# Kernel tuning notes

Hardware: AMD Instinct MI355X
Metric: run time of the kernel (lower is better)

## Reference

```python
import jax, jax.numpy as jnp
import numpy as np

HIDDEN_DIM = 2048
NUM_EXPERTS = 64
TOP_K = 8
NUM_TOKENS = 16384


def setup_inputs() -> dict:
    key = jax.random.key(0)
    k_x, k_w, k_b = jax.random.split(key, 3)
    X = jax.random.normal(k_x, (NUM_TOKENS, HIDDEN_DIM), dtype=jnp.float32)
    # nn.Linear(hidden_dim, num_experts): weight [out, in], bias [out]
    bound = 1.0 / np.sqrt(HIDDEN_DIM)
    W_gate = jax.random.uniform(k_w, (NUM_EXPERTS, HIDDEN_DIM), jnp.float32, -bound, bound)
    b_gate = jax.random.uniform(k_b, (NUM_EXPERTS,), jnp.float32, -bound, bound)
    return {"X": X, "W_gate": W_gate, "b_gate": b_gate}


def reference(X, W_gate, b_gate):
    # gate linear: [T, H] @ [H, E] + [E] -> [T, E]
    router_logits = jnp.einsum('th,eh->te', X, W_gate) + b_gate
    # softmax in float32 (matches dtype=torch.float)
    router_probs = jax.nn.softmax(router_logits.astype(jnp.float32), axis=-1)
    # top-k over experts: [T, K]
    router_weights, selected_experts_indices = jax.lax.top_k(router_probs, TOP_K)
    router_weights = router_weights / jnp.sum(router_weights, axis=-1, keepdims=True)
    router_weights = router_weights.astype(X.dtype)
    # one-hot [T, K, E] -> permute(2,1,0) -> [E, K, T]
    expert_mask = jax.nn.one_hot(selected_experts_indices, NUM_EXPERTS, dtype=jnp.int64 if jax.config.jax_enable_x64 else jnp.int32)
    expert_mask = jnp.transpose(expert_mask, (2, 1, 0))
    return (router_logits, router_weights, selected_experts_indices.astype(jnp.int32), expert_mask)
```

## Files before the change

kernel.cpp:

```cpp
#include <hip/hip_runtime.h>

#define NT 16384
#define NH 2048
#define NE 64
#define TOPK 8
#define TT 64
#define KC 64
#define NCH (NH / KC)

#define LOFF 0
#define WOFF (NT * NE)
#define IOFF (WOFF + NT * TOPK)
#define MOFF (IOFF + NT * TOPK)

typedef __attribute__((ext_vector_type(8))) short short8;
typedef __attribute__((ext_vector_type(4))) float floatx4;

union FragU { uint4 u; short8 s; };

__device__ __forceinline__ unsigned pack3(float a, float b, unsigned& w1, unsigned& w2) {
    unsigned au = __float_as_uint(a), bu = __float_as_uint(b);
    unsigned ah0 = au & 0xFFFF0000u, bh0 = bu & 0xFFFF0000u;
    float ra = a - __uint_as_float(ah0);
    float rb = b - __uint_as_float(bh0);
    unsigned ar = __float_as_uint(ra), br = __float_as_uint(rb);
    unsigned ah1 = ar & 0xFFFF0000u, bh1 = br & 0xFFFF0000u;
    float sa = ra - __uint_as_float(ah1);
    float sb = rb - __uint_as_float(bh1);
    w1 = bh1 | (ah1 >> 16);
    w2 = (__float_as_uint(sb) & 0xFFFF0000u) | (__float_as_uint(sa) >> 16);
    return bh0 | (ah0 >> 16);
}

__global__ __launch_bounds__(512, 1)
void router_kernel(const float* __restrict__ X, const float* __restrict__ Wg,
                   const float* __restrict__ bg, float* __restrict__ out) {
    __shared__ unsigned short SP[2][6][64][64];
    __shared__ float P[64 * 64];
    __shared__ float Ls[TT][NE + 1];

    const int tid  = threadIdx.x;
    const int wave = tid >> 6;
    const int l    = tid & 63;
    const int tp = wave & 1, ep = (wave >> 1) & 1, kh = wave >> 2;
    const int tbase = blockIdx.x * TT;

    const int srow = tid >> 3;
    const int g8   = tid & 7;
    const int spg  = g8 ^ (srow & 7);
    const float* xrow = X  + (size_t)(tbase + srow) * NH + g8 * 8;
    const float* wrow = Wg + (size_t)srow * NH + g8 * 8;

    const int lr = l & 15, lq = l >> 4;

    floatx4 acc[2][2];
#pragma unroll
    for (int a = 0; a < 2; a++)
#pragma unroll
        for (int b = 0; b < 2; b++) acc[a][b] = (floatx4)0.0f;

    float4 xl0 = *(const float4*)(xrow);
    float4 xl1 = *(const float4*)(xrow + 4);
    float4 wl0 = *(const float4*)(wrow);
    float4 wl1 = *(const float4*)(wrow + 4);

    for (int k = 0; k < NCH; k++) {
        const int bsel = k & 1;
        unsigned xw1[4], xw2[4], ww1[4], ww2[4];
        uint4 x0, w0, x1, x2, w1v, w2v;
        x0.x = pack3(xl0.x, xl0.y, xw1[0], xw2[0]);
        x0.y = pack3(xl0.z, xl0.w, xw1[1], xw2[1]);
        x0.z = pack3(xl1.x, xl1.y, xw1[2], xw2[2]);
        x0.w = pack3(xl1.z, xl1.w, xw1[3], xw2[3]);
        w0.x = pack3(wl0.x, wl0.y, ww1[0], ww2[0]);
        w0.y = pack3(wl0.z, wl0.w, ww1[1], ww2[1]);
        w0.z = pack3(wl1.x, wl1.y, ww1[2], ww2[2]);
        w0.w = pack3(wl1.z, wl1.w, ww1[3], ww2[3]);
        x1 = make_uint4(xw1[0], xw1[1], xw1[2], xw1[3]);
        x2 = make_uint4(xw2[0], xw2[1], xw2[2], xw2[3]);
        w1v = make_uint4(ww1[0], ww1[1], ww1[2], ww1[3]);
        w2v = make_uint4(ww2[0], ww2[1], ww2[2], ww2[3]);
        *(uint4*)&SP[bsel][0][srow][spg * 8] = x0;
        *(uint4*)&SP[bsel][1][srow][spg * 8] = x1;
        *(uint4*)&SP[bsel][2][srow][spg * 8] = x2;
        *(uint4*)&SP[bsel][3][srow][spg * 8] = w0;
        *(uint4*)&SP[bsel][4][srow][spg * 8] = w1v;
        *(uint4*)&SP[bsel][5][srow][spg * 8] = w2v;
        __syncthreads();

        if (k + 1 < NCH) {
            const int go = (k + 1) * KC;
            xl0 = *(const float4*)(xrow + go);
            xl1 = *(const float4*)(xrow + go + 4);
            wl0 = *(const float4*)(wrow + go);
            wl1 = *(const float4*)(wrow + go + 4);
        }

        if ((k >> 4) == kh) {
#pragma unroll
            for (int s = 0; s < 2; s++) {
                short8 af[2][3], bf[2][3];
#pragma unroll
                for (int a = 0; a < 2; a++) {
                    const int row = (tp * 2 + a) * 16 + lr;
                    const int pgr = (s * 4 + lq) ^ (lr & 7);
#pragma unroll
                    for (int p = 0; p < 3; p++) {
                        FragU t; t.u = *(const uint4*)&SP[bsel][p][row][pgr * 8];
                        af[a][p] = t.s;
                    }
                }
#pragma unroll
                for (int b = 0; b < 2; b++) {
                    const int row = (ep * 2 + b) * 16 + lr;
                    const int pgr = (s * 4 + lq) ^ (lr & 7);
#pragma unroll
                    for (int p = 0; p < 3; p++) {
                        FragU t; t.u = *(const uint4*)&SP[bsel][3 + p][row][pgr * 8];
                        bf[b][p] = t.s;
                    }
                }
#pragma unroll
                for (int a = 0; a < 2; a++)
#pragma unroll
                    for (int b = 0; b < 2; b++) {
                        acc[a][b] = __builtin_amdgcn_mfma_f32_16x16x32_bf16(af[a][0], bf[b][0], acc[a][b], 0, 0, 0);
                        acc[a][b] = __builtin_amdgcn_mfma_f32_16x16x32_bf16(af[a][0], bf[b][1], acc[a][b], 0, 0, 0);
                        acc[a][b] = __builtin_amdgcn_mfma_f32_16x16x32_bf16(af[a][1], bf[b][0], acc[a][b], 0, 0, 0);
                        acc[a][b] = __builtin_amdgcn_mfma_f32_16x16x32_bf16(af[a][1], bf[b][1], acc[a][b], 0, 0, 0);
                        acc[a][b] = __builtin_amdgcn_mfma_f32_16x16x32_bf16(af[a][0], bf[b][2], acc[a][b], 0, 0, 0);
                        acc[a][b] = __builtin_amdgcn_mfma_f32_16x16x32_bf16(af[a][2], bf[b][0], acc[a][b], 0, 0, 0);
                    }
            }
        }
    }
    __syncthreads();

    if (kh == 1) {
#pragma unroll
        for (int a = 0; a < 2; a++)
#pragma unroll
            for (int b = 0; b < 2; b++)
#pragma unroll
                for (int r = 0; r < 4; r++) {
                    const int tok = (tp * 2 + a) * 16 + lq * 4 + r;
                    const int exp = (ep * 2 + b) * 16 + lr;
                    P[tok * 64 + exp] = acc[a][b][r];
                }
    }
    __syncthreads();

    if (kh == 0) {
#pragma unroll
        for (int b = 0; b < 2; b++) {
            const int exp = (ep * 2 + b) * 16 + lr;
            const float bias = bg[exp];
#pragma unroll
            for (int a = 0; a < 2; a++)
#pragma unroll
                for (int r = 0; r < 4; r++) {
                    const int tok = (tp * 2 + a) * 16 + lq * 4 + r;
                    Ls[tok][exp] = acc[a][b][r] + P[tok * 64 + exp] + bias;
                }
        }
    } else {
        float4 z = make_float4(0.f, 0.f, 0.f, 0.f);
        for (int m = tid - 256; m < 8192; m += 256) {
            int seg = m >> 4;
            int off = (m & 15) << 2;
            *(float4*)(out + MOFF + (size_t)seg * NT + tbase + off) = z;
        }
    }
    __syncthreads();

#pragma unroll
    for (int v = 0; v < 2; v++) {
        int f  = v * 512 + tid;
        int t  = f >> 4;
        int c4 = (f & 15) << 2;
        float4 o = make_float4(Ls[t][c4], Ls[t][c4 + 1], Ls[t][c4 + 2], Ls[t][c4 + 3]);
        *(float4*)(out + LOFF + (size_t)(tbase + t) * NE + c4) = o;
    }

    if (tid < TT) {
        const int t = tid;
        const size_t gt = (size_t)(tbase + t);

        float m = -1e30f;
#pragma unroll
        for (int e = 0; e < NE; e++) m = fmaxf(m, Ls[t][e]);

        unsigned long long sel = 0ULL;
        int   idxs[TOPK];
        float vals[TOPK];
#pragma unroll
        for (int kk = 0; kk < TOPK; kk++) {
            float best = -1e30f;
            int   bi   = 0;
            for (int e = 0; e < NE; e++) {
                if (!((sel >> e) & 1ULL)) {
                    float v = Ls[t][e];
                    if (v > best) { best = v; bi = e; }
                }
            }
            sel |= (1ULL << bi);
            idxs[kk] = bi;
            vals[kk] = best;
        }

        float ex[TOPK];
        float s = 0.0f;
#pragma unroll
        for (int kk = 0; kk < TOPK; kk++) { ex[kk] = __expf(vals[kk] - m); s += ex[kk]; }
        float inv = 1.0f / s;

#pragma unroll
        for (int kk = 0; kk < TOPK; kk++) {
            out[WOFF + gt * TOPK + kk] = ex[kk] * inv;
            out[IOFF + gt * TOPK + kk] = (float)idxs[kk];
            out[MOFF + (size_t)idxs[kk] * (TOPK * NT) + (size_t)kk * NT + gt] = 1.0f;
        }
    }
}

extern "C" void kernel_launch(void* const* d_in, const int* in_sizes, int n_in,
                              void* d_out, int out_size, void* d_ws, size_t ws_size,
                              hipStream_t stream) {
    const float* X  = (const float*)d_in[0];
    const float* Wg = (const float*)d_in[1];
    const float* bg = (const float*)d_in[2];
    float* out = (float*)d_out;

    hipLaunchKernelGGL(router_kernel, dim3(NT / TT), dim3(512), 0, stream,
                       X, Wg, bg, out);
}
```

Before: 238.1 us.

## Pre-split gate weights into bf16x3 fragments and load MFMA operands directly from global

Adds a small pre-kernel that converts W_gate once per call into MFMA-fragment-ordered bf16 triple-split form in workspace. The main kernel now uses 32-token blocks of 256 threads with a four-way K split. Each wave loads X and the pre-split W fragments straight from global into registers, with no LDS staging or per-chunk barriers, and reduces partial sums through shared memory. Top-k moves from a serial per-thread loop to 8-lane shuffle reductions. The cost is an extra kernel launch and heavier per-wave global traffic for W, which is shared across blocks and expected to hit in cache.

```diff
diff --git a/kernel.cpp b/kernel.cpp
--- a/kernel.cpp
+++ b/kernel.cpp
@@ -4,9 +4,11 @@
 #define NH 2048
 #define NE 64
 #define TOPK 8
-#define TT 64
-#define KC 64
-#define NCH (NH / KC)
+
+#define TB 32
+#define KSTEPS 64
+#define KQ 4
+#define KSW (KSTEPS / KQ)
 
 #define LOFF 0
 #define WOFF (NT * NE)
@@ -32,195 +34,183 @@
     return bh0 | (ah0 >> 16);
 }
 
-__global__ __launch_bounds__(512, 1)
-void router_kernel(const float* __restrict__ X, const float* __restrict__ Wg,
+__global__ __launch_bounds__(64)
+void wconv_kernel(const float* __restrict__ Wg, uint4* __restrict__ wsp) {
+    const int b = blockIdx.x;
+    const int t = b >> 2, g = b & 3;
+    const int l = threadIdx.x;
+    const int e  = g * 16 + (l & 15);
+    const int k0 = t * 32 + (l >> 4) * 8;
+    const float* src = Wg + (size_t)e * NH + k0;
+    float4 w0 = *(const float4*)src;
+    float4 w1 = *(const float4*)(src + 4);
+    unsigned u1[4], u2[4];
+    uint4 p0;
+    p0.x = pack3(w0.x, w0.y, u1[0], u2[0]);
+    p0.y = pack3(w0.z, w0.w, u1[1], u2[1]);
+    p0.z = pack3(w1.x, w1.y, u1[2], u2[2]);
+    p0.w = pack3(w1.z, w1.w, u1[3], u2[3]);
+    uint4* dst = wsp + (size_t)((t * 4 + g) * 3) * 64 + l;
+    dst[0]   = p0;
+    dst[64]  = make_uint4(u1[0], u1[1], u1[2], u1[3]);
+    dst[128] = make_uint4(u2[0], u2[1], u2[2], u2[3]);
+}
+
+__global__ __launch_bounds__(256, 2)
+void router_kernel(const float* __restrict__ X, const uint4* __restrict__ wsp,
                    const float* __restrict__ bg, float* __restrict__ out) {
-    __shared__ unsigned short SP[2][6][64][64];
-    __shared__ float P[64 * 64];
-    __shared__ float Ls[TT][NE + 1];
-
-    const int tid  = threadIdx.x;
-    const int wave = tid >> 6;
-    const int l    = tid & 63;
-    const int tp = wave & 1, ep = (wave >> 1) & 1, kh = wave >> 2;
-    const int tbase = blockIdx.x * TT;
-
-    const int srow = tid >> 3;
-    const int g8   = tid & 7;
-    const int spg  = g8 ^ (srow & 7);
-    const float* xrow = X  + (size_t)(tbase + srow) * NH + g8 * 8;
-    const float* wrow = Wg + (size_t)srow * NH + g8 * 8;
-
-    const int lr = l & 15, lq = l >> 4;
-
-    floatx4 acc[2][2];
+    __shared__ __align__(16) float P[KQ][TB][68];
+    __shared__ __align__(16) float Ls[TB][68];
+
+    const int tid = threadIdx.x;
+    const int kh  = tid >> 6;
+    const int l   = tid & 63;
+    const int lr  = l & 15, lq = l >> 4;
+    const int tbase = blockIdx.x * TB;
+
+    floatx4 acc[2][4];
 #pragma unroll
     for (int a = 0; a < 2; a++)
 #pragma unroll
-        for (int b = 0; b < 2; b++) acc[a][b] = (floatx4)0.0f;
-
-    float4 xl0 = *(const float4*)(xrow);
-    float4 xl1 = *(const float4*)(xrow + 4);
-    float4 wl0 = *(const float4*)(wrow);
-    float4 wl1 = *(const float4*)(wrow + 4);
-
-    for (int k = 0; k < NCH; k++) {
-        const int bsel = k & 1;
-        unsigned xw1[4], xw2[4], ww1[4], ww2[4];
-        uint4 x0, w0, x1, x2, w1v, w2v;
-        x0.x = pack3(xl0.x, xl0.y, xw1[0], xw2[0]);
-        x0.y = pack3(xl0.z, xl0.w, xw1[1], xw2[1]);
-        x0.z = pack3(xl1.x, xl1.y, xw1[2], xw2[2]);
-        x0.w = pack3(xl1.z, xl1.w, xw1[3], xw2[3]);
-        w0.x = pack3(wl0.x, wl0.y, ww1[0], ww2[0]);
-        w0.y = pack3(wl0.z, wl0.w, ww1[1], ww2[1]);
-        w0.z = pack3(wl1.x, wl1.y, ww1[2], ww2[2]);
-        w0.w = pack3(wl1.z, wl1.w, ww1[3], ww2[3]);
-        x1 = make_uint4(xw1[0], xw1[1], xw1[2], xw1[3]);
-        x2 = make_uint4(xw2[0], xw2[1], xw2[2], xw2[3]);
-        w1v = make_uint4(ww1[0], ww1[1], ww1[2], ww1[3]);
-        w2v = make_uint4(ww2[0], ww2[1], ww2[2], ww2[3]);
-        *(uint4*)&SP[bsel][0][srow][spg * 8] = x0;
-        *(uint4*)&SP[bsel][1][srow][spg * 8] = x1;
-        *(uint4*)&SP[bsel][2][srow][spg * 8] = x2;
-        *(uint4*)&SP[bsel][3][srow][spg * 8] = w0;
-        *(uint4*)&SP[bsel][4][srow][spg * 8] = w1v;
-        *(uint4*)&SP[bsel][5][srow][spg * 8] = w2v;
-        __syncthreads();
-
-        if (k + 1 < NCH) {
-            const int go = (k + 1) * KC;
-            xl0 = *(const float4*)(xrow + go);
-            xl1 = *(const float4*)(xrow + go + 4);
-            wl0 = *(const float4*)(wrow + go);
-            wl1 = *(const float4*)(wrow + go + 4);
-        }
-
-        if ((k >> 4) == kh) {
-#pragma unroll
-            for (int s = 0; s < 2; s++) {
-                short8 af[2][3], bf[2][3];
-#pragma unroll
-                for (int a = 0; a < 2; a++) {
-                    const int row = (tp * 2 + a) * 16 + lr;
-                    const int pgr = (s * 4 + lq) ^ (lr & 7);
-#pragma unroll
-                    for (int p = 0; p < 3; p++) {
-                        FragU t; t.u = *(const uint4*)&SP[bsel][p][row][pgr * 8];
-                        af[a][p] = t.s;
-                    }
-                }
-#pragma unroll
-                for (int b = 0; b < 2; b++) {
-                    const int row = (ep * 2 + b) * 16 + lr;
-                    const int pgr = (s * 4 + lq) ^ (lr & 7);
-#pragma unroll
-                    for (int p = 0; p < 3; p++) {
-                        FragU t; t.u = *(const uint4*)&SP[bsel][3 + p][row][pgr * 8];
-                        bf[b][p] = t.s;
-                    }
-                }
-#pragma unroll
-                for (int a = 0; a < 2; a++)
-#pragma unroll
-                    for (int b = 0; b < 2; b++) {
-                        acc[a][b] = __builtin_amdgcn_mfma_f32_16x16x32_bf16(af[a][0], bf[b][0], acc[a][b], 0, 0, 0);
-                        acc[a][b] = __builtin_amdgcn_mfma_f32_16x16x32_bf16(af[a][0], bf[b][1], acc[a][b], 0, 0, 0);
-                        acc[a][b] = __builtin_amdgcn_mfma_f32_16x16x32_bf16(af[a][1], bf[b][0], acc[a][b], 0, 0, 0);
-                        acc[a][b] = __builtin_amdgcn_mfma_f32_16x16x32_bf16(af[a][1], bf[b][1], acc[a][b], 0, 0, 0);
-                        acc[a][b] = __builtin_amdgcn_mfma_f32_16x16x32_bf16(af[a][0], bf[b][2], acc[a][b], 0, 0, 0);
-                        acc[a][b] = __builtin_amdgcn_mfma_f32_16x16x32_bf16(af[a][2], bf[b][0], acc[a][b], 0, 0, 0);
-                    }
+        for (int g = 0; g < 4; g++) acc[a][g] = (floatx4)0.0f;
+
+    const float* xp0 = X + (size_t)(tbase + lr) * NH + kh * (KSW * 32) + lq * 8;
+    const float* xp1 = xp0 + (size_t)16 * NH;
+    const uint4* wp = wsp + (size_t)(kh * KSW) * 12 * 64 + l;
+
+    float4 a0lo = *(const float4*)xp0;
+    float4 a0hi = *(const float4*)(xp0 + 4);
+    float4 a1lo = *(const float4*)xp1;
+    float4 a1hi = *(const float4*)(xp1 + 4);
+
+    {
+        float4 z = make_float4(0.f, 0.f, 0.f, 0.f);
+#pragma unroll
+        for (int m = 0; m < 16; m++) {
+            int f2  = tid + 256 * m;
+            int seg = f2 >> 3;
+            int off = (f2 & 7) << 2;
+            *(float4*)(out + MOFF + (size_t)seg * NT + tbase + off) = z;
+        }
+    }
+
+#pragma unroll 2
+    for (int t = 0; t < KSW; t++) {
+        FragU b[4][3];
+        const uint4* wt = wp + t * 768;
+#pragma unroll
+        for (int g = 0; g < 4; g++)
+#pragma unroll
+            for (int p = 0; p < 3; p++)
+                b[g][p].u = wt[(g * 3 + p) * 64];
+
+        FragU af[2][3];
+        {
+            unsigned u1[4], u2[4];
+            uint4 q;
+            q.x = pack3(a0lo.x, a0lo.y, u1[0], u2[0]);
+            q.y = pack3(a0lo.z, a0lo.w, u1[1], u2[1]);
+            q.z = pack3(a0hi.x, a0hi.y, u1[2], u2[2]);
+            q.w = pack3(a0hi.z, a0hi.w, u1[3], u2[3]);
+            af[0][0].u = q;
+            af[0][1].u = make_uint4(u1[0], u1[1], u1[2], u1[3]);
+            af[0][2].u = make_uint4(u2[0], u2[1], u2[2], u2[3]);
+            q.x = pack3(a1lo.x, a1lo.y, u1[0], u2[0]);
+            q.y = pack3(a1lo.z, a1lo.w, u1[1], u2[1]);
+            q.z = pack3(a1hi.x, a1hi.y, u1[2], u2[2]);
+            q.w = pack3(a1hi.z, a1hi.w, u1[3], u2[3]);
+            af[1][0].u = q;
+            af[1][1].u = make_uint4(u1[0], u1[1], u1[2], u1[3]);
+            af[1][2].u = make_uint4(u2[0], u2[1], u2[2], u2[3]);
+        }
+
+        if (t + 1 < KSW) {
+            const float* nx0 = xp0 + (t + 1) * 32;
+            const float* nx1 = xp1 + (t + 1) * 32;
+            a0lo = *(const float4*)nx0;
+            a0hi = *(const float4*)(nx0 + 4);
+            a1lo = *(const float4*)nx1;
+            a1hi = *(const float4*)(nx1 + 4);
+        }
+
+#pragma unroll
+        for (int g = 0; g < 4; g++)
+#pragma unroll
+            for (int a = 0; a < 2; a++) {
+                acc[a][g] = __builtin_amdgcn_mfma_f32_16x16x32_bf16(af[a][0].s, b[g][0].s, acc[a][g], 0, 0, 0);
+                acc[a][g] = __builtin_amdgcn_mfma_f32_16x16x32_bf16(af[a][0].s, b[g][1].s, acc[a][g], 0, 0, 0);
+                acc[a][g] = __builtin_amdgcn_mfma_f32_16x16x32_bf16(af[a][1].s, b[g][0].s, acc[a][g], 0, 0, 0);
+                acc[a][g] = __builtin_amdgcn_mfma_f32_16x16x32_bf16(af[a][1].s, b[g][1].s, acc[a][g], 0, 0, 0);
+                acc[a][g] = __builtin_amdgcn_mfma_f32_16x16x32_bf16(af[a][0].s, b[g][2].s, acc[a][g], 0, 0, 0);
+                acc[a][g] = __builtin_amdgcn_mfma_f32_16x16x32_bf16(af[a][2].s, b[g][0].s, acc[a][g], 0, 0, 0);
             }
-        }
-    }
+    }
+
+#pragma unroll
+    for (int a = 0; a < 2; a++)
+#pragma unroll
+        for (int g = 0; g < 4; g++)
+#pragma unroll
+            for (int r = 0; r < 4; r++)
+                P[kh][a * 16 + lq * 4 + r][g * 16 + lr] = acc[a][g][r];
     __syncthreads();
 
-    if (kh == 1) {
-#pragma unroll
-        for (int a = 0; a < 2; a++)
-#pragma unroll
-            for (int b = 0; b < 2; b++)
-#pragma unroll
-                for (int r = 0; r < 4; r++) {
-                    const int tok = (tp * 2 + a) * 16 + lq * 4 + r;
-                    const int exp = (ep * 2 + b) * 16 + lr;
-                    P[tok * 64 + exp] = acc[a][b][r];
-                }
+#pragma unroll
+    for (int jj = 0; jj < 2; jj++) {
+        int f4  = tid + 256 * jj;
+        int tok = f4 >> 4;
+        int e4  = (f4 & 15) << 2;
+        float4 s0 = *(float4*)&P[0][tok][e4];
+        float4 s1 = *(float4*)&P[1][tok][e4];
+        float4 s2 = *(float4*)&P[2][tok][e4];
+        float4 s3 = *(float4*)&P[3][tok][e4];
+        float4 bb = *(const float4*)(bg + e4);
+        float4 v;
+        v.x = s0.x + s1.x + s2.x + s3.x + bb.x;
+        v.y = s0.y + s1.y + s2.y + s3.y + bb.y;
+        v.z = s0.z + s1.z + s2.z + s3.z + bb.z;
+        v.w = s0.w + s1.w + s2.w + s3.w + bb.w;
+        *(float4*)&Ls[tok][e4] = v;
+        *(float4*)(out + LOFF + (size_t)tbase * NE + (size_t)f4 * 4) = v;
     }
     __syncthreads();
 
-    if (kh == 0) {
-#pragma unroll
-        for (int b = 0; b < 2; b++) {
-            const int exp = (ep * 2 + b) * 16 + lr;
-            const float bias = bg[exp];
-#pragma unroll
-            for (int a = 0; a < 2; a++)
-#pragma unroll
-                for (int r = 0; r < 4; r++) {
-                    const int tok = (tp * 2 + a) * 16 + lq * 4 + r;
-                    Ls[tok][exp] = acc[a][b][r] + P[tok * 64 + exp] + bias;
-                }
-        }
-    } else {
-        float4 z = make_float4(0.f, 0.f, 0.f, 0.f);
-        for (int m = tid - 256; m < 8192; m += 256) {
-            int seg = m >> 4;
-            int off = (m & 15) << 2;
-            *(float4*)(out + MOFF + (size_t)seg * NT + tbase + off) = z;
-        }
-    }
-    __syncthreads();
-
-#pragma unroll
-    for (int v = 0; v < 2; v++) {
-        int f  = v * 512 + tid;
-        int t  = f >> 4;
-        int c4 = (f & 15) << 2;
-        float4 o = make_float4(Ls[t][c4], Ls[t][c4 + 1], Ls[t][c4 + 2], Ls[t][c4 + 3]);
-        *(float4*)(out + LOFF + (size_t)(tbase + t) * NE + c4) = o;
-    }
-
-    if (tid < TT) {
-        const int t = tid;
-        const size_t gt = (size_t)(tbase + t);
-
-        float m = -1e30f;
-#pragma unroll
-        for (int e = 0; e < NE; e++) m = fmaxf(m, Ls[t][e]);
-
-        unsigned long long sel = 0ULL;
-        int   idxs[TOPK];
-        float vals[TOPK];
-#pragma unroll
-        for (int kk = 0; kk < TOPK; kk++) {
-            float best = -1e30f;
-            int   bi   = 0;
-            for (int e = 0; e < NE; e++) {
-                if (!((sel >> e) & 1ULL)) {
-                    float v = Ls[t][e];
-                    if (v > best) { best = v; bi = e; }
-                }
-            }
-            sel |= (1ULL << bi);
-            idxs[kk] = bi;
-            vals[kk] = best;
-        }
-
-        float ex[TOPK];
-        float s = 0.0f;
-#pragma unroll
-        for (int kk = 0; kk < TOPK; kk++) { ex[kk] = __expf(vals[kk] - m); s += ex[kk]; }
-        float inv = 1.0f / s;
-
-#pragma unroll
-        for (int kk = 0; kk < TOPK; kk++) {
-            out[WOFF + gt * TOPK + kk] = ex[kk] * inv;
-            out[IOFF + gt * TOPK + kk] = (float)idxs[kk];
-            out[MOFF + (size_t)idxs[kk] * (TOPK * NT) + (size_t)kk * NT + gt] = 1.0f;
-        }
-    }
+    const int tok = (tid >> 6) * 8 + ((tid & 63) >> 3);
+    const int el  = tid & 7;
+    float4 va = *(float4*)&Ls[tok][el * 8];
+    float4 vb = *(float4*)&Ls[tok][el * 8 + 4];
+    float v[8] = {va.x, va.y, va.z, va.w, vb.x, vb.y, vb.z, vb.w};
+
+    unsigned msk = 0;
+    float m0 = 0.f, ssum = 0.f, myv = 0.f;
+    int myi = 0;
+#pragma unroll
+    for (int r = 0; r < 8; r++) {
+        float bv = -3.0e38f; int bi = 64;
+#pragma unroll
+        for (int j = 0; j < 8; j++) {
+            bool better = (((msk >> j) & 1u) == 0u) && (v[j] > bv);
+            bv = better ? v[j] : bv;
+            bi = better ? (el * 8 + j) : bi;
+        }
+#pragma unroll
+        for (int s2 = 1; s2 < 8; s2 <<= 1) {
+            float ov = __shfl_xor(bv, s2);
+            int   oi = __shfl_xor(bi, s2);
+            bool take = (ov > bv) || (ov == bv && oi < bi);
+            bv = take ? ov : bv;
+            bi = take ? oi : bi;
+        }
+        if ((bi >> 3) == el) msk |= (1u << (bi & 7));
+        if (r == 0) m0 = bv;
+        ssum += __expf(bv - m0);
+        if (r == el) { myv = bv; myi = bi; }
+    }
+    float w = __expf(myv - m0) / ssum;
+    size_t gt = (size_t)(tbase + tok);
+    out[WOFF + gt * TOPK + el] = w;
+    out[IOFF + gt * TOPK + el] = (float)myi;
+    out[MOFF + (size_t)myi * (TOPK * NT) + (size_t)el * NT + gt] = 1.0f;
 }
 
 extern "C" void kernel_launch(void* const* d_in, const int* in_sizes, int n_in,
@@ -230,7 +220,9 @@
     const float* Wg = (const float*)d_in[1];
     const float* bg = (const float*)d_in[2];
     float* out = (float*)d_out;
-
-    hipLaunchKernelGGL(router_kernel, dim3(NT / TT), dim3(512), 0, stream,
-                       X, Wg, bg, out);
-}
+    uint4* wsp = (uint4*)d_ws;
+
+    hipLaunchKernelGGL(wconv_kernel, dim3(KSTEPS * 4), dim3(64), 0, stream, Wg, wsp);
+    hipLaunchKernelGGL(router_kernel, dim3(NT / TB), dim3(256), 0, stream,
+                       X, (const uint4*)wsp, bg, out);
+}
```

New measurement: 223.2 us. -6.3%, faster.
